# Kernel tuning notes

Measured on AMD Instinct MI355X. Metric: run time of the kernel, lower is better.

## Reference

```python
import jax, jax.numpy as jnp
import numpy as np

N, E, D_IN, D_OUT = 50000, 800000, 128, 128


def setup_inputs() -> dict:
    key = jax.random.key(0)
    ks = jax.random.split(key, 4)
    x = jax.random.normal(ks[0], (N, D_IN), jnp.float32)
    edge_index = jax.random.randint(ks[1], (2, E), 0, N)
    # GCNConv.lin weight (no bias in lin; bias added after aggregation)
    W = jax.random.normal(ks[2], (D_IN, D_OUT), jnp.float32) / np.sqrt(D_IN)
    b = jnp.zeros((D_OUT,), jnp.float32)
    # edge_weight_predictor: Linear(2*dim_in, 1)
    w_pred = jax.random.normal(ks[3], (2 * D_IN, 1), jnp.float32) / np.sqrt(2 * D_IN)
    b_pred = jnp.zeros((1,), jnp.float32)
    return {"x": x, "edge_index": edge_index, "W": W, "b": b,
            "w_pred": w_pred, "b_pred": b_pred}


def reference(x, edge_index, W, b, w_pred, b_pred):
    n = x.shape[0]
    src, tgt = edge_index[0], edge_index[1]

    # --- learned edge weights: gather, concat, linear, sigmoid ---
    eemb = jnp.concatenate([x[src], x[tgt]], axis=1)          # [E, 2D]
    ew = jax.nn.sigmoid(eemb @ w_pred + b_pred)[:, 0]         # [E]

    # --- GCNConv with edge_weight (PyG gcn_norm: add self-loops w=1) ---
    loop = jnp.arange(n)
    row = jnp.concatenate([src, loop])                        # message sources
    col = jnp.concatenate([tgt, loop])                        # aggregation targets
    w_full = jnp.concatenate([ew, jnp.ones((n,), ew.dtype)])

    deg = jax.ops.segment_sum(w_full, col, num_segments=n)    # weighted in-degree
    dis = jnp.where(deg > 0, jax.lax.rsqrt(deg), 0.0)         # deg^{-1/2}, inf->0
    norm = dis[row] * w_full * dis[col]                       # [E+N]

    xw = x @ W                                                # [N, D_OUT]
    msg = norm[:, None] * xw[row]                             # [E+N, D_OUT]
    out = jax.ops.segment_sum(msg, col, num_segments=n) + b   # [N, D_OUT]
    return out
```

## Files before the change

### kernel.cpp

```cpp
#include <hip/hip_runtime.h>
#include <math.h>

#define D 128
#define NC 32

typedef __attribute__((ext_vector_type(8))) short bf16x8;
typedef __attribute__((ext_vector_type(4))) float f32x4;

__device__ __forceinline__ unsigned int bf16_round(float f) {
  unsigned int u = __float_as_uint(f);
  return (u + 0x7fffu + ((u >> 16) & 1u)) >> 16;
}
__device__ __forceinline__ float bf_lo(unsigned int u) { return __uint_as_float(u << 16); }
__device__ __forceinline__ float bf_hi(unsigned int u) { return __uint_as_float(u & 0xffff0000u); }

__global__ __launch_bounds__(256) void k_pre(const float* __restrict__ x,
                                             const float* __restrict__ w_pred,
                                             const float* __restrict__ W,
                                             const int* __restrict__ tgt,
                                             float* __restrict__ p, float* __restrict__ q,
                                             unsigned int* __restrict__ xbh,
                                             unsigned short* __restrict__ wt,
                                             int* __restrict__ rank,
                                             int* __restrict__ partial,
                                             int n, int E, int nbHist, int total) {
  int bid = blockIdx.x;
  long long h0 = (long long)bid * nbHist / total;
  long long h1 = (long long)(bid + 1) * nbHist / total;
  if (h1 != h0) {
    int e = (int)h0 * 256 + threadIdx.x;
    if (e < E) {
      int t = tgt[e];
      int c = (e >> 8) & (NC - 1);
      rank[e] = atomicAdd(&partial[c * n + t], 1);
    }
    return;
  }
  int pqIdx = bid - (int)h1;
  int ptid = pqIdx * 256 + threadIdx.x;
  if (ptid < 16384) {
    int col = ptid >> 7, k = ptid & 127;
    wt[col * 128 + k] = (unsigned short)bf16_round(W[k * 128 + col]);
  }
  int wid = ptid >> 6;
  int lane = threadIdx.x & 63;
  if (wid >= n) return;
  float2 xv = ((const float2*)(x + (size_t)wid * D))[lane];
  xbh[(size_t)wid * 64 + lane] = bf16_round(xv.x) | (bf16_round(xv.y) << 16);
  float2 wp = ((const float2*)w_pred)[lane];
  float2 wq = ((const float2*)w_pred)[64 + lane];
  float pp = xv.x * wp.x + xv.y * wp.y;
  float qq = xv.x * wq.x + xv.y * wq.y;
#pragma unroll
  for (int off = 32; off > 0; off >>= 1) {
    pp += __shfl_down(pp, off);
    qq += __shfl_down(qq, off);
  }
  if (lane == 0) { p[wid] = pp; q[wid] = qq; }
}

__global__ __launch_bounds__(256) void k_scan1(const int* __restrict__ partial,
                                               int* __restrict__ rowptr,
                                               int* __restrict__ bsum, int n) {
  __shared__ int wsum[4];
  int base = blockIdx.x * 1024 + threadIdx.x * 4;
  int4 v = make_int4(0, 0, 0, 0);
  if (base + 3 < n) {
#pragma unroll
    for (int c = 0; c < NC; ++c) {
      int4 t = *(const int4*)(partial + (size_t)c * n + base);
      v.x += t.x; v.y += t.y; v.z += t.z; v.w += t.w;
    }
  } else {
#pragma unroll
    for (int c = 0; c < NC; ++c) {
      const int* pc = partial + (size_t)c * n;
      if (base + 0 < n) v.x += pc[base + 0];
      if (base + 1 < n) v.y += pc[base + 1];
      if (base + 2 < n) v.z += pc[base + 2];
      if (base + 3 < n) v.w += pc[base + 3];
    }
  }
  int s = v.x + v.y + v.z + v.w;
  int lane = threadIdx.x & 63;
  int wave = threadIdx.x >> 6;
  int incl = s;
#pragma unroll
  for (int off = 1; off < 64; off <<= 1) {
    int t = __shfl_up(incl, off);
    if (lane >= off) incl += t;
  }
  if (lane == 63) wsum[wave] = incl;
  __syncthreads();
  int woff = 0;
#pragma unroll
  for (int w = 0; w < 4; ++w) if (w < wave) woff += wsum[w];
  int excl = woff + incl - s;
  if (base + 0 < n) rowptr[base + 0] = excl;
  if (base + 1 < n) rowptr[base + 1] = excl + v.x;
  if (base + 2 < n) rowptr[base + 2] = excl + v.x + v.y;
  if (base + 3 < n) rowptr[base + 3] = excl + v.x + v.y + v.z;
  if (threadIdx.x == 255) bsum[blockIdx.x] = woff + incl;
}

__global__ __launch_bounds__(256) void k_cursors(int* __restrict__ rowptr,
                                                 const int* __restrict__ bsum,
                                                 const int* __restrict__ partial,
                                                 int* __restrict__ cursor,
                                                 int n, int E, int nb) {
  __shared__ int bpre_s[64];
  if (threadIdx.x < 64) {
    int lane = threadIdx.x;
    int v = (lane < nb) ? bsum[lane] : 0;
    int incl = v;
#pragma unroll
    for (int off = 1; off < 64; off <<= 1) {
      int t = __shfl_up(incl, off);
      if (lane >= off) incl += t;
    }
    bpre_s[lane] = incl - v;
  }
  __syncthreads();
  int t = blockIdx.x * blockDim.x + threadIdx.x;
  if (t < n) {
    int r = rowptr[t] + bpre_s[t >> 10];
    rowptr[t] = r;
#pragma unroll
    for (int c = 0; c < NC; ++c) {
      cursor[c * n + t] = r;
      r += partial[c * n + t];
    }
  }
  if (t == 0) rowptr[n] = E;
}

__global__ __launch_bounds__(256) void k_fill(const int* __restrict__ src,
                                              const int* __restrict__ tgt,
                                              const int* __restrict__ rank,
                                              const int* __restrict__ cursor,
                                              const float* __restrict__ p,
                                              const float* __restrict__ q,
                                              const float* __restrict__ b_pred,
                                              unsigned int* __restrict__ edata,
                                              int E, int n) {
  int e = blockIdx.x * blockDim.x + threadIdx.x;
  if (e >= E) return;
  int s = src[e], t = tgt[e];
  int c = (e >> 8) & (NC - 1);
  int pos = cursor[c * n + t] + rank[e];
  float z = p[s] + q[t] + b_pred[0];
  float w = 1.0f / (1.0f + expf(-z));
  edata[pos] = (unsigned int)s | (bf16_round(w) << 16);
}

__global__ __launch_bounds__(256) void k_gemm_mfma(const short* __restrict__ xbh,
                                                   const short* __restrict__ wt,
                                                   const int* __restrict__ rowptr,
                                                   const unsigned int* __restrict__ edata,
                                                   float* __restrict__ dis,
                                                   unsigned int* __restrict__ xwh, int n) {
  __shared__ float cbuf[4][16 * 128];
  int wave = threadIdx.x >> 6;
  int lane = threadIdx.x & 63;
  int row0 = blockIdx.x * 64 + wave * 16;

  int rr = lane >> 2, jj = lane & 3;
  int grow = row0 + rr;
  float dv = 0.0f;
  if (grow < n) {
    int beg = rowptr[grow], end = rowptr[grow + 1];
    float sum = 0.0f;
    for (int j = beg + jj; j < end; j += 4) sum += bf_hi(edata[j]);
    sum += __shfl_xor(sum, 1);
    sum += __shfl_xor(sum, 2);
    float d = 1.0f + sum;
    dv = (d > 0.0f) ? rsqrtf(d) : 0.0f;
    if (jj == 0) dis[grow] = dv;
  }

  int rA = lane & 15, quad = lane >> 4;
  f32x4 acc[8];
#pragma unroll
  for (int cb = 0; cb < 8; ++cb) acc[cb] = (f32x4){0.f, 0.f, 0.f, 0.f};

  const short* arow = xbh + (size_t)(row0 + rA) * 128 + quad * 8;
  bool arow_ok = (row0 + rA) < n;
#pragma unroll
  for (int kk = 0; kk < 4; ++kk) {
    bf16x8 a;
    if (arow_ok) a = *(const bf16x8*)(arow + kk * 32);
    else a = (bf16x8){0, 0, 0, 0, 0, 0, 0, 0};
#pragma unroll
    for (int cb = 0; cb < 8; ++cb) {
      bf16x8 bf = *(const bf16x8*)(wt + (size_t)(cb * 16 + rA) * 128 + kk * 32 + quad * 8);
      acc[cb] = __builtin_amdgcn_mfma_f32_16x16x32_bf16(a, bf, acc[cb], 0, 0, 0);
    }
  }

#pragma unroll
  for (int cb = 0; cb < 8; ++cb)
#pragma unroll
    for (int r = 0; r < 4; ++r)
      cbuf[wave][(quad * 4 + r) * 128 + cb * 16 + rA] = acc[cb][r];
  __syncthreads();

  int ch = jj * 32;
  if (grow < n) {
    const float* cr = &cbuf[wave][rr * 128 + ch];
#pragma unroll
    for (int g = 0; g < 2; ++g) {
      uint4 o;
      o.x = bf16_round(cr[g * 16 + 0] * dv)  | (bf16_round(cr[g * 16 + 1] * dv) << 16);
      o.y = bf16_round(cr[g * 16 + 2] * dv)  | (bf16_round(cr[g * 16 + 3] * dv) << 16);
      o.z = bf16_round(cr[g * 16 + 4] * dv)  | (bf16_round(cr[g * 16 + 5] * dv) << 16);
      o.w = bf16_round(cr[g * 16 + 6] * dv)  | (bf16_round(cr[g * 16 + 7] * dv) << 16);
      uint4 o2;
      o2.x = bf16_round(cr[g * 16 + 8] * dv)  | (bf16_round(cr[g * 16 + 9] * dv) << 16);
      o2.y = bf16_round(cr[g * 16 + 10] * dv) | (bf16_round(cr[g * 16 + 11] * dv) << 16);
      o2.z = bf16_round(cr[g * 16 + 12] * dv) | (bf16_round(cr[g * 16 + 13] * dv) << 16);
      o2.w = bf16_round(cr[g * 16 + 14] * dv) | (bf16_round(cr[g * 16 + 15] * dv) << 16);
      *(uint4*)(xwh + (size_t)grow * 64 + (ch >> 1) + g * 8)     = o;
      *(uint4*)(xwh + (size_t)grow * 64 + (ch >> 1) + g * 8 + 4) = o2;
    }
  }
}

__global__ __launch_bounds__(256) void k_gather(const int* __restrict__ rowptr,
                                                const unsigned int* __restrict__ edata,
                                                const uint4* __restrict__ xwh4,
                                                const float* __restrict__ dis,
                                                const float* __restrict__ b,
                                                float* __restrict__ out, int n) {
  int wid = (blockIdx.x * blockDim.x + threadIdx.x) >> 6;
  int lane = threadIdx.x & 63;
  if (wid >= n) return;
  int cj = lane & 15;
  int rg = lane >> 4;
  int2 rp = *(const int2*)(rowptr + wid);
  int beg = rp.x, end = rp.y;

  float acc[8];
  if (rg == 0) {
    uint4 v = xwh4[(size_t)wid * 16 + cj];
    acc[0] = bf_lo(v.x); acc[1] = bf_hi(v.x);
    acc[2] = bf_lo(v.y); acc[3] = bf_hi(v.y);
    acc[4] = bf_lo(v.z); acc[5] = bf_hi(v.z);
    acc[6] = bf_lo(v.w); acc[7] = bf_hi(v.w);
  } else {
#pragma unroll
    for (int i = 0; i < 8; ++i) acc[i] = 0.0f;
  }

  for (int j0 = beg; j0 < end; j0 += 64) {
    int m = end - j0; if (m > 64) m = 64;
    unsigned int wl = 0;
    if (lane < m) wl = edata[j0 + lane];
    for (int k = 0; k < m; k += 16) {
      unsigned int w0 = (unsigned int)__shfl((int)wl, k + rg);
      unsigned int w1 = (unsigned int)__shfl((int)wl, k + 4 + rg);
      unsigned int w2 = (unsigned int)__shfl((int)wl, k + 8 + rg);
      unsigned int w3 = (unsigned int)__shfl((int)wl, k + 12 + rg);
      if (k + rg >= m)      w0 = 0;
      if (k + 4 + rg >= m)  w1 = 0;
      if (k + 8 + rg >= m)  w2 = 0;
      if (k + 12 + rg >= m) w3 = 0;
      uint4 v0 = xwh4[(size_t)(w0 & 0xffffu) * 16 + cj];
      uint4 v1 = xwh4[(size_t)(w1 & 0xffffu) * 16 + cj];
      uint4 v2 = xwh4[(size_t)(w2 & 0xffffu) * 16 + cj];
      uint4 v3 = xwh4[(size_t)(w3 & 0xffffu) * 16 + cj];
      float c0 = bf_hi(w0), c1 = bf_hi(w1), c2 = bf_hi(w2), c3 = bf_hi(w3);
      acc[0] = fmaf(c0, bf_lo(v0.x), acc[0]); acc[1] = fmaf(c0, bf_hi(v0.x), acc[1]);
      acc[2] = fmaf(c0, bf_lo(v0.y), acc[2]); acc[3] = fmaf(c0, bf_hi(v0.y), acc[3]);
      acc[4] = fmaf(c0, bf_lo(v0.z), acc[4]); acc[5] = fmaf(c0, bf_hi(v0.z), acc[5]);
      acc[6] = fmaf(c0, bf_lo(v0.w), acc[6]); acc[7] = fmaf(c0, bf_hi(v0.w), acc[7]);
      acc[0] = fmaf(c1, bf_lo(v1.x), acc[0]); acc[1] = fmaf(c1, bf_hi(v1.x), acc[1]);
      acc[2] = fmaf(c1, bf_lo(v1.y), acc[2]); acc[3] = fmaf(c1, bf_hi(v1.y), acc[3]);
      acc[4] = fmaf(c1, bf_lo(v1.z), acc[4]); acc[5] = fmaf(c1, bf_hi(v1.z), acc[5]);
      acc[6] = fmaf(c1, bf_lo(v1.w), acc[6]); acc[7] = fmaf(c1, bf_hi(v1.w), acc[7]);
      acc[0] = fmaf(c2, bf_lo(v2.x), acc[0]); acc[1] = fmaf(c2, bf_hi(v2.x), acc[1]);
      acc[2] = fmaf(c2, bf_lo(v2.y), acc[2]); acc[3] = fmaf(c2, bf_hi(v2.y), acc[3]);
      acc[4] = fmaf(c2, bf_lo(v2.z), acc[4]); acc[5] = fmaf(c2, bf_hi(v2.z), acc[5]);
      acc[6] = fmaf(c2, bf_lo(v2.w), acc[6]); acc[7] = fmaf(c2, bf_hi(v2.w), acc[7]);
      acc[0] = fmaf(c3, bf_lo(v3.x), acc[0]); acc[1] = fmaf(c3, bf_hi(v3.x), acc[1]);
      acc[2] = fmaf(c3, bf_lo(v3.y), acc[2]); acc[3] = fmaf(c3, bf_hi(v3.y), acc[3]);
      acc[4] = fmaf(c3, bf_lo(v3.z), acc[4]); acc[5] = fmaf(c3, bf_hi(v3.z), acc[5]);
      acc[6] = fmaf(c3, bf_lo(v3.w), acc[6]); acc[7] = fmaf(c3, bf_hi(v3.w), acc[7]);
    }
  }

#pragma unroll
  for (int i = 0; i < 8; ++i) {
    acc[i] += __shfl_xor(acc[i], 16);
    acc[i] += __shfl_xor(acc[i], 32);
  }

  if (rg == 0) {
    float dt = dis[wid];
    float4 b0 = ((const float4*)b)[cj * 2];
    float4 b1 = ((const float4*)b)[cj * 2 + 1];
    float4 o0, o1;
    o0.x = fmaf(dt, acc[0], b0.x); o0.y = fmaf(dt, acc[1], b0.y);
    o0.z = fmaf(dt, acc[2], b0.z); o0.w = fmaf(dt, acc[3], b0.w);
    o1.x = fmaf(dt, acc[4], b1.x); o1.y = fmaf(dt, acc[5], b1.y);
    o1.z = fmaf(dt, acc[6], b1.z); o1.w = fmaf(dt, acc[7], b1.w);
    ((float4*)out)[(size_t)wid * 32 + cj * 2] = o0;
    ((float4*)out)[(size_t)wid * 32 + cj * 2 + 1] = o1;
  }
}

extern "C" void kernel_launch(void* const* d_in, const int* in_sizes, int n_in,
                              void* d_out, int out_size, void* d_ws, size_t ws_size,
                              hipStream_t stream) {
  const float* x      = (const float*)d_in[0];
  const int*   ei     = (const int*)d_in[1];
  const float* W      = (const float*)d_in[2];
  const float* b      = (const float*)d_in[3];
  const float* w_pred = (const float*)d_in[4];
  const float* b_pred = (const float*)d_in[5];

  int n = in_sizes[0] / D;
  int E = in_sizes[1] / 2;
  const int* src = ei;
  const int* tgt = ei + E;

  float* out = (float*)d_out;
  float* ws  = (float*)d_ws;
  unsigned int* xwh = (unsigned int*)ws;
  unsigned int* xbh = xwh + (size_t)n * 64;
  float* p       = (float*)(xbh + (size_t)n * 64);
  float* q       = p + n;
  float* dis     = q + n;
  unsigned int* edata = (unsigned int*)(dis + n);
  int*   rank    = (int*)(edata + E);
  int*   partial = rank + E;
  int*   cursor  = partial + (size_t)NC * n;
  int*   rowptr  = cursor + (size_t)NC * n;
  int*   bsum    = rowptr + n + 1;
  unsigned short* wt = (unsigned short*)(bsum + 64);

  int nb = (n + 1023) / 1024;
  int nbPq = (n + 3) / 4;
  int nbHist = (E + 255) / 256;
  int total = nbPq + nbHist;

  (void)hipMemsetAsync(partial, 0, (size_t)NC * n * sizeof(int), stream);
  k_pre<<<total, 256, 0, stream>>>(x, w_pred, W, tgt, p, q, xbh, wt, rank, partial,
                                   n, E, nbHist, total);
  k_scan1<<<nb, 256, 0, stream>>>(partial, rowptr, bsum, n);
  k_cursors<<<(n + 255) / 256, 256, 0, stream>>>(rowptr, bsum, partial, cursor, n, E, nb);
  k_fill<<<(E + 255) / 256, 256, 0, stream>>>(src, tgt, rank, cursor, p, q, b_pred, edata, E, n);
  k_gemm_mfma<<<(n + 63) / 64, 256, 0, stream>>>((const short*)xbh, (const short*)wt,
                                                 rowptr, edata, dis, xwh, n);
  k_gather<<<(n + 3) / 4, 256, 0, stream>>>(rowptr, edata, (const uint4*)xwh, dis, b, out, n);
}
```

Baseline: 193.8 us.

## Replace chunked rank-based CSR build with single counter and atomic cursor fill

The CSR construction drops the 32-way partitioned per-target histogram and per-edge rank array in favour of a single per-node counter. Edge slots are now claimed in the fill kernel with an atomic increment on each target's cursor. Weighted in-degree is accumulated with float atomics during the fill, so the GEMM kernel no longer walks edge lists. This removes the large memset and the 32x scan and cursor traffic. In exchange, edge order within a row becomes nondeterministic, float atomics add contention, and summation order varies between runs.

```diff
diff --git a/kernel.cpp b/kernel.cpp
--- a/kernel.cpp
+++ b/kernel.cpp
@@ -2,7 +2,6 @@
 #include <math.h>
 
 #define D 128
-#define NC 32
 
 typedef __attribute__((ext_vector_type(8))) short bf16x8;
 typedef __attribute__((ext_vector_type(4))) float f32x4;
@@ -21,19 +20,14 @@
                                              float* __restrict__ p, float* __restrict__ q,
                                              unsigned int* __restrict__ xbh,
                                              unsigned short* __restrict__ wt,
-                                             int* __restrict__ rank,
-                                             int* __restrict__ partial,
+                                             int* __restrict__ cnt,
                                              int n, int E, int nbHist, int total) {
   int bid = blockIdx.x;
   long long h0 = (long long)bid * nbHist / total;
   long long h1 = (long long)(bid + 1) * nbHist / total;
   if (h1 != h0) {
     int e = (int)h0 * 256 + threadIdx.x;
-    if (e < E) {
-      int t = tgt[e];
-      int c = (e >> 8) & (NC - 1);
-      rank[e] = atomicAdd(&partial[c * n + t], 1);
-    }
+    if (e < E) atomicAdd(&cnt[tgt[e]], 1);
     return;
   }
   int pqIdx = bid - (int)h1;
@@ -59,27 +53,19 @@
   if (lane == 0) { p[wid] = pp; q[wid] = qq; }
 }
 
-__global__ __launch_bounds__(256) void k_scan1(const int* __restrict__ partial,
+__global__ __launch_bounds__(256) void k_scan1(const int* __restrict__ cnt,
                                                int* __restrict__ rowptr,
                                                int* __restrict__ bsum, int n) {
   __shared__ int wsum[4];
   int base = blockIdx.x * 1024 + threadIdx.x * 4;
   int4 v = make_int4(0, 0, 0, 0);
   if (base + 3 < n) {
-#pragma unroll
-    for (int c = 0; c < NC; ++c) {
-      int4 t = *(const int4*)(partial + (size_t)c * n + base);
-      v.x += t.x; v.y += t.y; v.z += t.z; v.w += t.w;
-    }
+    v = *(const int4*)(cnt + base);
   } else {
-#pragma unroll
-    for (int c = 0; c < NC; ++c) {
-      const int* pc = partial + (size_t)c * n;
-      if (base + 0 < n) v.x += pc[base + 0];
-      if (base + 1 < n) v.y += pc[base + 1];
-      if (base + 2 < n) v.z += pc[base + 2];
-      if (base + 3 < n) v.w += pc[base + 3];
-    }
+    if (base + 0 < n) v.x = cnt[base + 0];
+    if (base + 1 < n) v.y = cnt[base + 1];
+    if (base + 2 < n) v.z = cnt[base + 2];
+    if (base + 3 < n) v.w = cnt[base + 3];
   }
   int s = v.x + v.y + v.z + v.w;
   int lane = threadIdx.x & 63;
@@ -105,7 +91,6 @@
 
 __global__ __launch_bounds__(256) void k_cursors(int* __restrict__ rowptr,
                                                  const int* __restrict__ bsum,
-                                                 const int* __restrict__ partial,
                                                  int* __restrict__ cursor,
                                                  int n, int E, int nb) {
   __shared__ int bpre_s[64];
@@ -125,38 +110,33 @@
   if (t < n) {
     int r = rowptr[t] + bpre_s[t >> 10];
     rowptr[t] = r;
-#pragma unroll
-    for (int c = 0; c < NC; ++c) {
-      cursor[c * n + t] = r;
-      r += partial[c * n + t];
-    }
+    cursor[t] = r;
   }
   if (t == 0) rowptr[n] = E;
 }
 
 __global__ __launch_bounds__(256) void k_fill(const int* __restrict__ src,
                                               const int* __restrict__ tgt,
-                                              const int* __restrict__ rank,
-                                              const int* __restrict__ cursor,
+                                              int* __restrict__ cursor,
                                               const float* __restrict__ p,
                                               const float* __restrict__ q,
                                               const float* __restrict__ b_pred,
                                               unsigned int* __restrict__ edata,
+                                              float* __restrict__ degw,
                                               int E, int n) {
   int e = blockIdx.x * blockDim.x + threadIdx.x;
   if (e >= E) return;
   int s = src[e], t = tgt[e];
-  int c = (e >> 8) & (NC - 1);
-  int pos = cursor[c * n + t] + rank[e];
   float z = p[s] + q[t] + b_pred[0];
   float w = 1.0f / (1.0f + expf(-z));
+  int pos = atomicAdd(&cursor[t], 1);
   edata[pos] = (unsigned int)s | (bf16_round(w) << 16);
+  atomicAdd(&degw[t], w);
 }
 
 __global__ __launch_bounds__(256) void k_gemm_mfma(const short* __restrict__ xbh,
                                                    const short* __restrict__ wt,
-                                                   const int* __restrict__ rowptr,
-                                                   const unsigned int* __restrict__ edata,
+                                                   const float* __restrict__ degw,
                                                    float* __restrict__ dis,
                                                    unsigned int* __restrict__ xwh, int n) {
   __shared__ float cbuf[4][16 * 128];
@@ -168,12 +148,7 @@
   int grow = row0 + rr;
   float dv = 0.0f;
   if (grow < n) {
-    int beg = rowptr[grow], end = rowptr[grow + 1];
-    float sum = 0.0f;
-    for (int j = beg + jj; j < end; j += 4) sum += bf_hi(edata[j]);
-    sum += __shfl_xor(sum, 1);
-    sum += __shfl_xor(sum, 2);
-    float d = 1.0f + sum;
+    float d = 1.0f + degw[grow];
     dv = (d > 0.0f) ? rsqrtf(d) : 0.0f;
     if (jj == 0) dis[grow] = dv;
   }
@@ -331,10 +306,10 @@
   float* q       = p + n;
   float* dis     = q + n;
   unsigned int* edata = (unsigned int*)(dis + n);
-  int*   rank    = (int*)(edata + E);
-  int*   partial = rank + E;
-  int*   cursor  = partial + (size_t)NC * n;
-  int*   rowptr  = cursor + (size_t)NC * n;
+  float* degw    = (float*)(edata + E);
+  int*   cnt     = (int*)(degw + n);
+  int*   cursor  = cnt + n;
+  int*   rowptr  = cursor + n;
   int*   bsum    = rowptr + n + 1;
   unsigned short* wt = (unsigned short*)(bsum + 64);
 
@@ -343,13 +318,13 @@
   int nbHist = (E + 255) / 256;
   int total = nbPq + nbHist;
 
-  (void)hipMemsetAsync(partial, 0, (size_t)NC * n * sizeof(int), stream);
-  k_pre<<<total, 256, 0, stream>>>(x, w_pred, W, tgt, p, q, xbh, wt, rank, partial,
+  (void)hipMemsetAsync(degw, 0, (size_t)2 * n * sizeof(int), stream);
+  k_pre<<<total, 256, 0, stream>>>(x, w_pred, W, tgt, p, q, xbh, wt, cnt,
                                    n, E, nbHist, total);
-  k_scan1<<<nb, 256, 0, stream>>>(partial, rowptr, bsum, n);
-  k_cursors<<<(n + 255) / 256, 256, 0, stream>>>(rowptr, bsum, partial, cursor, n, E, nb);
-  k_fill<<<(E + 255) / 256, 256, 0, stream>>>(src, tgt, rank, cursor, p, q, b_pred, edata, E, n);
+  k_scan1<<<nb, 256, 0, stream>>>(cnt, rowptr, bsum, n);
+  k_cursors<<<(n + 255) / 256, 256, 0, stream>>>(rowptr, bsum, cursor, n, E, nb);
+  k_fill<<<(E + 255) / 256, 256, 0, stream>>>(src, tgt, cursor, p, q, b_pred, edata, degw, E, n);
   k_gemm_mfma<<<(n + 63) / 64, 256, 0, stream>>>((const short*)xbh, (const short*)wt,
-                                                 rowptr, edata, dis, xwh, n);
+                                                 degw, dis, xwh, n);
   k_gather<<<(n + 3) / 4, 256, 0, stream>>>(rowptr, edata, (const uint4*)xwh, dis, b, out, n);
 }
```

New measurement: 251.3 us. 1.3x slower.

## Merge edge fill with XW GEMM in one launch and move degree normalization to gather

Applied to the files above, without the earlier changes.

The edge-fill kernel and the MFMA GEMM are combined into one launch whose blocks are split between the two jobs by index. This removes the GEMM's dependency on the filled CSR. Degree normalization is no longer applied to XW in the GEMM. A separate small kernel computes dis, and the gather applies the source and target dis factors per edge instead. This lets the GEMM overlap with the scatter fill, at the cost of an extra random dis load per edge in the gather and one more small launch.

```diff
diff --git a/kernel.cpp b/kernel.cpp
--- a/kernel.cpp
+++ b/kernel.cpp
@@ -134,49 +134,38 @@
   if (t == 0) rowptr[n] = E;
 }
 
-__global__ __launch_bounds__(256) void k_fill(const int* __restrict__ src,
-                                              const int* __restrict__ tgt,
-                                              const int* __restrict__ rank,
-                                              const int* __restrict__ cursor,
-                                              const float* __restrict__ p,
-                                              const float* __restrict__ q,
-                                              const float* __restrict__ b_pred,
-                                              unsigned int* __restrict__ edata,
-                                              int E, int n) {
-  int e = blockIdx.x * blockDim.x + threadIdx.x;
-  if (e >= E) return;
-  int s = src[e], t = tgt[e];
-  int c = (e >> 8) & (NC - 1);
-  int pos = cursor[c * n + t] + rank[e];
-  float z = p[s] + q[t] + b_pred[0];
-  float w = 1.0f / (1.0f + expf(-z));
-  edata[pos] = (unsigned int)s | (bf16_round(w) << 16);
-}
-
-__global__ __launch_bounds__(256) void k_gemm_mfma(const short* __restrict__ xbh,
-                                                   const short* __restrict__ wt,
-                                                   const int* __restrict__ rowptr,
-                                                   const unsigned int* __restrict__ edata,
-                                                   float* __restrict__ dis,
-                                                   unsigned int* __restrict__ xwh, int n) {
+__global__ __launch_bounds__(256) void k_fg(const int* __restrict__ src,
+                                            const int* __restrict__ tgt,
+                                            const int* __restrict__ rank,
+                                            const int* __restrict__ cursor,
+                                            const float* __restrict__ p,
+                                            const float* __restrict__ q,
+                                            const float* __restrict__ b_pred,
+                                            unsigned int* __restrict__ edata,
+                                            const short* __restrict__ xbh,
+                                            const short* __restrict__ wt,
+                                            unsigned int* __restrict__ xwh,
+                                            int E, int n, int nbFill, int total) {
   __shared__ float cbuf[4][16 * 128];
+  int bid = blockIdx.x;
+  long long h0 = (long long)bid * nbFill / total;
+  long long h1 = (long long)(bid + 1) * nbFill / total;
+  if (h1 != h0) {
+    int e = (int)h0 * 256 + threadIdx.x;
+    if (e < E) {
+      int s = src[e], t = tgt[e];
+      int c = (e >> 8) & (NC - 1);
+      int pos = cursor[c * n + t] + rank[e];
+      float z = p[s] + q[t] + b_pred[0];
+      float w = 1.0f / (1.0f + expf(-z));
+      edata[pos] = (unsigned int)s | (bf16_round(w) << 16);
+    }
+    return;
+  }
+  int gIdx = bid - (int)h1;
   int wave = threadIdx.x >> 6;
   int lane = threadIdx.x & 63;
-  int row0 = blockIdx.x * 64 + wave * 16;
-
-  int rr = lane >> 2, jj = lane & 3;
-  int grow = row0 + rr;
-  float dv = 0.0f;
-  if (grow < n) {
-    int beg = rowptr[grow], end = rowptr[grow + 1];
-    float sum = 0.0f;
-    for (int j = beg + jj; j < end; j += 4) sum += bf_hi(edata[j]);
-    sum += __shfl_xor(sum, 1);
-    sum += __shfl_xor(sum, 2);
-    float d = 1.0f + sum;
-    dv = (d > 0.0f) ? rsqrtf(d) : 0.0f;
-    if (jj == 0) dis[grow] = dv;
-  }
+  int row0 = gIdx * 64 + wave * 16;
 
   int rA = lane & 15, quad = lane >> 4;
   f32x4 acc[8];
@@ -204,24 +193,44 @@
       cbuf[wave][(quad * 4 + r) * 128 + cb * 16 + rA] = acc[cb][r];
   __syncthreads();
 
+  int rr = lane >> 2, jj = lane & 3;
+  int grow = row0 + rr;
   int ch = jj * 32;
   if (grow < n) {
     const float* cr = &cbuf[wave][rr * 128 + ch];
 #pragma unroll
     for (int g = 0; g < 2; ++g) {
       uint4 o;
-      o.x = bf16_round(cr[g * 16 + 0] * dv)  | (bf16_round(cr[g * 16 + 1] * dv) << 16);
-      o.y = bf16_round(cr[g * 16 + 2] * dv)  | (bf16_round(cr[g * 16 + 3] * dv) << 16);
-      o.z = bf16_round(cr[g * 16 + 4] * dv)  | (bf16_round(cr[g * 16 + 5] * dv) << 16);
-      o.w = bf16_round(cr[g * 16 + 6] * dv)  | (bf16_round(cr[g * 16 + 7] * dv) << 16);
+      o.x = bf16_round(cr[g * 16 + 0])  | (bf16_round(cr[g * 16 + 1]) << 16);
+      o.y = bf16_round(cr[g * 16 + 2])  | (bf16_round(cr[g * 16 + 3]) << 16);
+      o.z = bf16_round(cr[g * 16 + 4])  | (bf16_round(cr[g * 16 + 5]) << 16);
+      o.w = bf16_round(cr[g * 16 + 6])  | (bf16_round(cr[g * 16 + 7]) << 16);
       uint4 o2;
-      o2.x = bf16_round(cr[g * 16 + 8] * dv)  | (bf16_round(cr[g * 16 + 9] * dv) << 16);
-      o2.y = bf16_round(cr[g * 16 + 10] * dv) | (bf16_round(cr[g * 16 + 11] * dv) << 16);
-      o2.z = bf16_round(cr[g * 16 + 12] * dv) | (bf16_round(cr[g * 16 + 13] * dv) << 16);
-      o2.w = bf16_round(cr[g * 16 + 14] * dv) | (bf16_round(cr[g * 16 + 15] * dv) << 16);
+      o2.x = bf16_round(cr[g * 16 + 8])  | (bf16_round(cr[g * 16 + 9]) << 16);
+      o2.y = bf16_round(cr[g * 16 + 10]) | (bf16_round(cr[g * 16 + 11]) << 16);
+      o2.z = bf16_round(cr[g * 16 + 12]) | (bf16_round(cr[g * 16 + 13]) << 16);
+      o2.w = bf16_round(cr[g * 16 + 14]) | (bf16_round(cr[g * 16 + 15]) << 16);
       *(uint4*)(xwh + (size_t)grow * 64 + (ch >> 1) + g * 8)     = o;
       *(uint4*)(xwh + (size_t)grow * 64 + (ch >> 1) + g * 8 + 4) = o2;
     }
+  }
+}
+
+__global__ __launch_bounds__(256) void k_dis(const int* __restrict__ rowptr,
+                                             const unsigned int* __restrict__ edata,
+                                             float* __restrict__ dis, int n) {
+  int tid = blockIdx.x * 256 + threadIdx.x;
+  int grow = tid >> 2;
+  int jj = tid & 3;
+  if (grow >= n) return;
+  int beg = rowptr[grow], end = rowptr[grow + 1];
+  float sum = 0.0f;
+  for (int j = beg + jj; j < end; j += 4) sum += bf_hi(edata[j]);
+  sum += __shfl_xor(sum, 1);
+  sum += __shfl_xor(sum, 2);
+  if (jj == 0) {
+    float d = 1.0f + sum;
+    dis[grow] = (d > 0.0f) ? rsqrtf(d) : 0.0f;
   }
 }
 
@@ -236,16 +245,17 @@
   if (wid >= n) return;
   int cj = lane & 15;
   int rg = lane >> 4;
+  float dt = dis[wid];
   int2 rp = *(const int2*)(rowptr + wid);
   int beg = rp.x, end = rp.y;
 
   float acc[8];
   if (rg == 0) {
     uint4 v = xwh4[(size_t)wid * 16 + cj];
-    acc[0] = bf_lo(v.x); acc[1] = bf_hi(v.x);
-    acc[2] = bf_lo(v.y); acc[3] = bf_hi(v.y);
-    acc[4] = bf_lo(v.z); acc[5] = bf_hi(v.z);
-    acc[6] = bf_lo(v.w); acc[7] = bf_hi(v.w);
+    acc[0] = dt * bf_lo(v.x); acc[1] = dt * bf_hi(v.x);
+    acc[2] = dt * bf_lo(v.y); acc[3] = dt * bf_hi(v.y);
+    acc[4] = dt * bf_lo(v.z); acc[5] = dt * bf_hi(v.z);
+    acc[6] = dt * bf_lo(v.w); acc[7] = dt * bf_hi(v.w);
   } else {
 #pragma unroll
     for (int i = 0; i < 8; ++i) acc[i] = 0.0f;
@@ -268,7 +278,12 @@
       uint4 v1 = xwh4[(size_t)(w1 & 0xffffu) * 16 + cj];
       uint4 v2 = xwh4[(size_t)(w2 & 0xffffu) * 16 + cj];
       uint4 v3 = xwh4[(size_t)(w3 & 0xffffu) * 16 + cj];
-      float c0 = bf_hi(w0), c1 = bf_hi(w1), c2 = bf_hi(w2), c3 = bf_hi(w3);
+      float d0 = dis[w0 & 0xffffu];
+      float d1 = dis[w1 & 0xffffu];
+      float d2 = dis[w2 & 0xffffu];
+      float d3 = dis[w3 & 0xffffu];
+      float c0 = bf_hi(w0) * d0, c1 = bf_hi(w1) * d1;
+      float c2 = bf_hi(w2) * d2, c3 = bf_hi(w3) * d3;
       acc[0] = fmaf(c0, bf_lo(v0.x), acc[0]); acc[1] = fmaf(c0, bf_hi(v0.x), acc[1]);
       acc[2] = fmaf(c0, bf_lo(v0.y), acc[2]); acc[3] = fmaf(c0, bf_hi(v0.y), acc[3]);
       acc[4] = fmaf(c0, bf_lo(v0.z), acc[4]); acc[5] = fmaf(c0, bf_hi(v0.z), acc[5]);
@@ -295,7 +310,6 @@
   }
 
   if (rg == 0) {
-    float dt = dis[wid];
     float4 b0 = ((const float4*)b)[cj * 2];
     float4 b1 = ((const float4*)b)[cj * 2 + 1];
     float4 o0, o1;
@@ -341,15 +355,20 @@
   int nb = (n + 1023) / 1024;
   int nbPq = (n + 3) / 4;
   int nbHist = (E + 255) / 256;
-  int total = nbPq + nbHist;
+  int totalPre = nbPq + nbHist;
+
+  int nbFill = (E + 255) / 256;
+  int nbGemm = (n + 63) / 64;
+  int totalFg = nbFill + nbGemm;
 
   (void)hipMemsetAsync(partial, 0, (size_t)NC * n * sizeof(int), stream);
-  k_pre<<<total, 256, 0, stream>>>(x, w_pred, W, tgt, p, q, xbh, wt, rank, partial,
-                                   n, E, nbHist, total);
+  k_pre<<<totalPre, 256, 0, stream>>>(x, w_pred, W, tgt, p, q, xbh, wt, rank, partial,
+                                      n, E, nbHist, totalPre);
   k_scan1<<<nb, 256, 0, stream>>>(partial, rowptr, bsum, n);
   k_cursors<<<(n + 255) / 256, 256, 0, stream>>>(rowptr, bsum, partial, cursor, n, E, nb);
-  k_fill<<<(E + 255) / 256, 256, 0, stream>>>(src, tgt, rank, cursor, p, q, b_pred, edata, E, n);
-  k_gemm_mfma<<<(n + 63) / 64, 256, 0, stream>>>((const short*)xbh, (const short*)wt,
-                                                 rowptr, edata, dis, xwh, n);
+  k_fg<<<totalFg, 256, 0, stream>>>(src, tgt, rank, cursor, p, q, b_pred, edata,
+                                    (const short*)xbh, (const short*)wt, xwh,
+                                    E, n, nbFill, totalFg);
+  k_dis<<<(4 * n + 255) / 256, 256, 0, stream>>>(rowptr, edata, dis, n);
   k_gather<<<(n + 3) / 4, 256, 0, stream>>>(rowptr, edata, (const uint4*)xwh, dis, b, out, n);
 }
```

After: 193.1 us. About the same (-0.4%).
